# Performance work log

Measured on AMD Instinct MI355X. Metric: run time of the kernel, lower is better.

The kernel has to match this reference:

```python
import jax, jax.numpy as jnp
import numpy as np

GROUPS = 32
EPS = 1e-6

def group_norm(x, scale, bias):
    B, H, W, C = x.shape
    xg = x.reshape(B, H, W, GROUPS, C // GROUPS)
    mean = xg.mean(axis=(1, 2, 4), keepdims=True)
    var = xg.var(axis=(1, 2, 4), keepdims=True)
    xg = (xg - mean) * jax.lax.rsqrt(var + EPS)
    return xg.reshape(B, H, W, C) * scale + bias

def nin(x, w, b):
    # 1x1 dense over channel dim
    return jnp.einsum('bhwc,cd->bhwd', x, w) + b

def setup_inputs() -> dict:
    key = jax.random.key(0)
    ks = jax.random.split(key, 6)
    B, H, W, C = 8, 64, 64, 256
    s = 1.0 / np.sqrt(C)
    return {
        'x': jax.random.normal(ks[0], (B, H, W, C), jnp.float32),
        'gn_scale': jnp.ones((C,), jnp.float32),
        'gn_bias': jnp.zeros((C,), jnp.float32),
        'Wq': jax.random.normal(ks[1], (C, C), jnp.float32) * s,
        'bq': jnp.zeros((C,), jnp.float32),
        'Wk': jax.random.normal(ks[2], (C, C), jnp.float32) * s,
        'bk': jnp.zeros((C,), jnp.float32),
        'Wv': jax.random.normal(ks[3], (C, C), jnp.float32) * s,
        'bv': jnp.zeros((C,), jnp.float32),
        'Wf': jax.random.normal(ks[4], (C, C), jnp.float32) * s,
        'bf': jnp.zeros((C,), jnp.float32),
    }

def reference(x, gn_scale, gn_bias, Wq, bq, Wk, bk, Wv, bv, Wf, bf):
    B, H, W, C = x.shape
    h = group_norm(x, gn_scale, gn_bias)
    q = nin(h, Wq, bq)
    k = nin(h, Wk, bk)
    v = nin(h, Wv, bv)
    w = jnp.einsum('bhwc,bHWc->bhwHW', q, k) * (C ** -0.5)  # [B,H,W,H,W]
    w = jax.nn.softmax(w.reshape(B, H, W, H * W), axis=-1).reshape(B, H, W, H, W)
    h = jnp.einsum('bhwHW,bHWc->bhwc', w, v)
    h = nin(h, Wf, bf)
    return (x + h) / np.sqrt(2.0)  # skip_rescale=True
```

## Files before the change

### kernel.cpp

```cpp
#include <hip/hip_runtime.h>
#include <math.h>


typedef __attribute__((ext_vector_type(8))) short bf16x8;
typedef __attribute__((ext_vector_type(4))) float f32x4;
typedef __attribute__((ext_vector_type(16))) float f32x16;
typedef __attribute__((ext_vector_type(8))) int i32x8;
typedef unsigned short u16;
typedef unsigned char u8;
typedef __attribute__((address_space(3))) unsigned int lds_u32;
typedef __attribute__((address_space(1))) unsigned int glb_u32;

namespace {
constexpr int Bn = 8;
constexpr int Np = 4096;
constexpr int Cc = 256;
constexpr float kEps = 1e-6f;
constexpr float kRsqrt2 = 0.70710678118654752440f;
constexpr int kRows = Bn * Np;
}

__device__ __forceinline__ u16 f2b(float x) {
  unsigned int u = __float_as_uint(x);
  u += 0x7fffu + ((u >> 16) & 1u);
  return (u16)(u >> 16);
}

__device__ __forceinline__ u8 f2fp8(float x) {
  return (u8)(__builtin_amdgcn_cvt_pk_fp8_f32(x, x, 0, false) & 0xff);
}

__device__ __forceinline__ void stage16(const void* g, void* l) {
  __builtin_amdgcn_global_load_lds((const glb_u32*)g, (lds_u32*)l, 16, 0, 0);
}

union V8U {
  uint4 u[2];
  i32x8 v;
};

__global__ __launch_bounds__(256) void conv_w_k(
    const float* __restrict__ Wq, const float* __restrict__ Wk,
    const float* __restrict__ Wv, const float* __restrict__ Wf,
    u16* __restrict__ wsw) {
  const int w = blockIdx.x;
  const float* W = (w == 0) ? Wq : (w == 1) ? Wk : (w == 2) ? Wv : Wf;
  const int t = threadIdx.x;
  const int nt = t >> 7, r = t & 127;
  for (int c0 = 0; c0 < 32; ++c0) {
    const int c = blockIdx.y * 32 + c0;
    const float val = W[(size_t)c * Cc + t];
    const int kt = c >> 6, kk = c & 63;
    const size_t byte = (((size_t)(w * 8 + nt * 4 + kt)) << 14) +
                        (((r * 128 + kk * 2)) ^ ((r & 7) << 4));
    *(u16*)((char*)wsw + byte) = f2b(val);
  }
}

__global__ __launch_bounds__(256) void gn_stats_k(const float* __restrict__ x,
                                                  float* __restrict__ st) {
  const int bg = blockIdx.x;
  const int b = bg >> 5, g = bg & 31;
  const float* base = x + (size_t)b * Np * Cc + g * 8;
  float s = 0.f, ss = 0.f;
  for (int i = threadIdx.x; i < Np * 2; i += 256) {
    const int p = i >> 1, hh = (i & 1) * 4;
    const float4 v = *(const float4*)(base + (size_t)p * Cc + hh);
    s += v.x + v.y + v.z + v.w;
    ss += v.x * v.x + v.y * v.y + v.z * v.z + v.w * v.w;
  }
  __shared__ float red[8];
#pragma unroll
  for (int off = 32; off; off >>= 1) {
    s += __shfl_down(s, off);
    ss += __shfl_down(ss, off);
  }
  const int wid = threadIdx.x >> 6;
  if ((threadIdx.x & 63) == 0) { red[wid] = s; red[wid + 4] = ss; }
  __syncthreads();
  if (threadIdx.x == 0) {
    s = red[0] + red[1] + red[2] + red[3];
    ss = red[4] + red[5] + red[6] + red[7];
    const float mean = s * (1.f / 32768.f);
    const float var = ss * (1.f / 32768.f) - mean * mean;
    st[bg * 2] = mean;
    st[bg * 2 + 1] = rsqrtf(var + kEps);
  }
}

__global__ __launch_bounds__(256) void gn_apply_k(const float* __restrict__ x,
                                                  const float* __restrict__ st,
                                                  const float* __restrict__ gs,
                                                  const float* __restrict__ gb,
                                                  u16* __restrict__ hsw) {
  const int total = kRows * Cc / 4;
  for (int i = blockIdx.x * blockDim.x + threadIdx.x; i < total;
       i += gridDim.x * blockDim.x) {
    const int c4 = i & 63;
    const int p = i >> 6;
    const int b = p >> 12;
    const int g = c4 >> 1;
    const float mean = st[(b * 32 + g) * 2];
    const float rstd = st[(b * 32 + g) * 2 + 1];
    const float4 xv = ((const float4*)x)[i];
    const float4 sv = ((const float4*)gs)[c4];
    const float4 bv = ((const float4*)gb)[c4];
    ushort4 o;
    o.x = f2b((xv.x - mean) * rstd * sv.x + bv.x);
    o.y = f2b((xv.y - mean) * rstd * sv.y + bv.y);
    o.z = f2b((xv.z - mean) * rstd * sv.z + bv.z);
    o.w = f2b((xv.w - mean) * rstd * sv.w + bv.w);
    const int mt = p >> 7, r = p & 127;
    const int c = c4 * 4, kt = c >> 6, kk = c & 63;
    const size_t byte = (((size_t)(mt * 4 + kt)) << 14) +
                        (((r * 128 + kk * 2)) ^ ((r & 7) << 4));
    *(ushort4*)((char*)hsw + byte) = o;
  }
}

__global__ __launch_bounds__(256, 2) void gemm_k(
    const u16* __restrict__ A_sw, const u16* __restrict__ wsw,
    const float* __restrict__ bq, const float* __restrict__ bk,
    const float* __restrict__ bv, const float* __restrict__ bf,
    const float* __restrict__ x, u8* __restrict__ qg, u8* __restrict__ kg,
    u8* __restrict__ vtt, float* __restrict__ out, int mode_sel) {
  __shared__ __align__(16) u16 Al[2][8192], Bl[2][8192];
  const int mode = (mode_sel < 0) ? blockIdx.z : mode_sel;
  const int mt0 = blockIdx.x;
  const int nt0 = blockIdx.y;
  const int t = threadIdx.x;
  const int w = t >> 6, l = t & 63;
  const int wm = w >> 1, wn = w & 1;
  const int lr = l & 15, lg = l >> 4;
  f32x4 acc[4][4];
#pragma unroll
  for (int i = 0; i < 4; ++i)
#pragma unroll
    for (int j = 0; j < 4; ++j) acc[i][j] = (f32x4){0.f, 0.f, 0.f, 0.f};

  auto stg = [&](int kt, int nxt) {
    const char* at = (const char*)A_sw + (((size_t)mt0 * 4 + kt) << 14);
    const char* bt =
        (const char*)wsw + (((size_t)(mode * 8 + nt0 * 4 + kt)) << 14);
    char* ad = (char*)&Al[nxt][0];
    char* bd = (char*)&Bl[nxt][0];
#pragma unroll
    for (int p = 0; p < 4; ++p) {
      const int c = p * 256 + t;
      stage16(at + c * 16, ad + c * 16);
      stage16(bt + c * 16, bd + c * 16);
    }
  };

  stg(0, 0);
  __syncthreads();
  for (int kt = 0; kt < 4; ++kt) {
    if (kt < 3) stg(kt + 1, (kt + 1) & 1);
    const char* Ac = (const char*)&Al[kt & 1][0];
    const char* Bc = (const char*)&Bl[kt & 1][0];
    __builtin_amdgcn_s_setprio(1);
#pragma unroll
    for (int ks = 0; ks < 2; ++ks) {
      bf16x8 af[4], bfr[4];
#pragma unroll
      for (int i = 0; i < 4; ++i)
        af[i] = *(const bf16x8*)(
            Ac + (((wm * 64 + i * 16 + lr) * 128 + ks * 64 + lg * 16) ^
                  ((lr & 7) << 4)));
#pragma unroll
      for (int j = 0; j < 4; ++j)
        bfr[j] = *(const bf16x8*)(
            Bc + (((wn * 64 + j * 16 + lr) * 128 + ks * 64 + lg * 16) ^
                  ((lr & 7) << 4)));
#pragma unroll
      for (int i = 0; i < 4; ++i)
#pragma unroll
        for (int j = 0; j < 4; ++j)
          acc[i][j] = __builtin_amdgcn_mfma_f32_16x16x32_bf16(af[i], bfr[j],
                                                              acc[i][j], 0, 0, 0);
    }
    __builtin_amdgcn_s_setprio(0);
    __syncthreads();
  }
  const int m0 = mt0 * 128 + wm * 64;
  const int n0 = nt0 * 128 + wn * 64;
  const float* bias = (mode == 0) ? bq : (mode == 1) ? bk : (mode == 2) ? bv : bf;
  float bv4[4];
#pragma unroll
  for (int j = 0; j < 4; ++j) bv4[j] = bias[n0 + j * 16 + lr];
#pragma unroll
  for (int i = 0; i < 4; ++i)
#pragma unroll
    for (int e = 0; e < 4; ++e) {
      const int m = m0 + i * 16 + lg * 4 + e;
#pragma unroll
      for (int j = 0; j < 4; ++j) {
        const int n = n0 + j * 16 + lr;
        const float val = acc[i][j][e] + bv4[j];
        if (mode == 0) {
          qg[(size_t)m * Cc + n] = f2fp8(val);
        } else if (mode == 1) {
          const size_t pos = ((size_t)(m >> 6)) * 16384 +
                             ((size_t)((m >> 5) & 1)) * 8192 +
                             (n >> 6) * 2048 +
                             ((m & 31) + 32 * ((n >> 5) & 1)) * 32 + (n & 31);
          kg[pos] = f2fp8(val);
        } else if (mode == 2) {
          const int kv = m & 63;
          const size_t pos = ((size_t)(m >> 6)) * 16384 + (n >> 5) * 2048 +
                             ((n & 31) + 32 * ((kv >> 2) & 1)) * 32 +
                             (kv & 3) + 4 * ((kv & 31) >> 3) + 16 * (kv >> 5);
          vtt[pos] = f2fp8(val);
        } else {
          out[(size_t)m * Cc + n] =
              (x[(size_t)m * Cc + n] + val) * kRsqrt2;
        }
      }
    }
}

__global__ __launch_bounds__(64, 1) void attn_mfma_k(
    const u8* __restrict__ qg, const u8* __restrict__ ksw,
    const u8* __restrict__ vsw, u16* __restrict__ h2) {
  const int id = blockIdx.x;
  const int b = id & 7;
  const int qt = id >> 3;
  const int l = threadIdx.x;
  const int lq = l & 31;
  const int hi = l >> 5;

  const u8* kbase = ksw + (size_t)b * Np * Cc;
  const u8* vbase = vsw + (size_t)b * Np * Cc;

  uint4 QF[4][2];
  {
    const u8* qrow = qg + ((size_t)b * Np + qt * 32 + lq) * Cc;
#pragma unroll
    for (int m = 0; m < 4; ++m) {
      QF[m][0] = *(const uint4*)(qrow + m * 64 + hi * 32);
      QF[m][1] = *(const uint4*)(qrow + m * 64 + hi * 32 + 16);
    }
  }
  f32x16 oacc[8];
#pragma unroll
  for (int nb = 0; nb < 8; ++nb)
#pragma unroll
    for (int r = 0; r < 16; ++r) oacc[nb][r] = 0.f;
  float lrow = 0.f;

  uint4 KR[2][4][2];
  uint4 VR[8][2];

  auto loadK = [&](int gt) {
    const u8* kt = kbase + (size_t)gt * 16384;
#pragma unroll
    for (int s = 0; s < 2; ++s)
#pragma unroll
      for (int m = 0; m < 4; ++m) {
        const u8* p = kt + s * 8192 + m * 2048 + l * 32;
        KR[s][m][0] = *(const uint4*)(p);
        KR[s][m][1] = *(const uint4*)(p + 16);
      }
  };
  auto loadV = [&](int gt) {
    const u8* vt = vbase + (size_t)gt * 16384;
#pragma unroll
    for (int cb = 0; cb < 8; ++cb) {
      const u8* p = vt + cb * 2048 + l * 32;
      VR[cb][0] = *(const uint4*)(p);
      VR[cb][1] = *(const uint4*)(p + 16);
    }
  };

  loadK(0);
  loadV(0);

  for (int t = 0; t < 64; ++t) {
    f32x16 s0, s1;
#pragma unroll
    for (int r = 0; r < 16; ++r) { s0[r] = 0.f; s1[r] = 0.f; }
    __builtin_amdgcn_s_setprio(1);
#pragma unroll
    for (int m = 0; m < 4; ++m) {
      V8U ka, kb, qv;
      ka.u[0] = KR[0][m][0]; ka.u[1] = KR[0][m][1];
      kb.u[0] = KR[1][m][0]; kb.u[1] = KR[1][m][1];
      qv.u[0] = QF[m][0]; qv.u[1] = QF[m][1];
      s0 = __builtin_amdgcn_mfma_scale_f32_32x32x64_f8f6f4(
          ka.v, qv.v, s0, 0, 0, 0, 0x7F, 0, 0x7F);
      s1 = __builtin_amdgcn_mfma_scale_f32_32x32x64_f8f6f4(
          kb.v, qv.v, s1, 0, 0, 0, 0x7F, 0, 0x7F);
    }
    __builtin_amdgcn_s_setprio(0);
    if (t < 63) loadK(t + 1);
    float p0[16], p1[16];
#pragma unroll
    for (int r = 0; r < 16; ++r) {
      p0[r] = __expf(s0[r] * 0.0625f - 2.0f);
      p1[r] = __expf(s1[r] * 0.0625f - 2.0f);
    }
    lrow += ((((p0[0] + p0[1]) + (p0[2] + p0[3])) +
              ((p0[4] + p0[5]) + (p0[6] + p0[7]))) +
             (((p0[8] + p0[9]) + (p0[10] + p0[11])) +
              ((p0[12] + p0[13]) + (p0[14] + p0[15]))));
    lrow += ((((p1[0] + p1[1]) + (p1[2] + p1[3])) +
              ((p1[4] + p1[5]) + (p1[6] + p1[7]))) +
             (((p1[8] + p1[9]) + (p1[10] + p1[11])) +
              ((p1[12] + p1[13]) + (p1[14] + p1[15]))));
    V8U PP;
    unsigned int d[8];
#pragma unroll
    for (int g = 0; g < 4; ++g) {
      unsigned int r0 = (unsigned int)__builtin_amdgcn_cvt_pk_fp8_f32(
          p0[4 * g + 0], p0[4 * g + 1], 0, false);
      d[g] = (unsigned int)__builtin_amdgcn_cvt_pk_fp8_f32(
          p0[4 * g + 2], p0[4 * g + 3], (int)r0, true);
      unsigned int r1 = (unsigned int)__builtin_amdgcn_cvt_pk_fp8_f32(
          p1[4 * g + 0], p1[4 * g + 1], 0, false);
      d[4 + g] = (unsigned int)__builtin_amdgcn_cvt_pk_fp8_f32(
          p1[4 * g + 2], p1[4 * g + 3], (int)r1, true);
    }
    PP.u[0] = make_uint4(d[0], d[1], d[2], d[3]);
    PP.u[1] = make_uint4(d[4], d[5], d[6], d[7]);
    __builtin_amdgcn_s_setprio(1);
#pragma unroll
    for (int cb = 0; cb < 8; ++cb) {
      V8U vv;
      vv.u[0] = VR[cb][0]; vv.u[1] = VR[cb][1];
      oacc[cb] = __builtin_amdgcn_mfma_scale_f32_32x32x64_f8f6f4(
          vv.v, PP.v, oacc[cb], 0, 0, 0, 0x7F, 0, 0x7F);
    }
    __builtin_amdgcn_s_setprio(0);
    if (t < 63) loadV(t + 1);
  }

  lrow += __shfl_xor(lrow, 32);
  const float inv = 1.f / lrow;
  const size_t mt = (size_t)b * 32 + (qt >> 2);
  const int r = (qt & 3) * 32 + lq;
#pragma unroll
  for (int nb = 0; nb < 8; ++nb)
#pragma unroll
    for (int g = 0; g < 4; ++g) {
      const int c = nb * 32 + g * 8 + hi * 4;
      const int kt = c >> 6, kk = c & 63;
      ushort4 val;
      val.x = f2b(oacc[nb][4 * g + 0] * inv);
      val.y = f2b(oacc[nb][4 * g + 1] * inv);
      val.z = f2b(oacc[nb][4 * g + 2] * inv);
      val.w = f2b(oacc[nb][4 * g + 3] * inv);
      const size_t byte =
          ((mt * 4 + kt) << 14) + (((r * 128 + kk * 2)) ^ ((r & 7) << 4));
      *(ushort4*)((char*)h2 + byte) = val;
    }
}

extern "C" void kernel_launch(void* const* d_in, const int* in_sizes, int n_in,
                              void* d_out, int out_size, void* d_ws,
                              size_t ws_size, hipStream_t stream) {
  const float* x = (const float*)d_in[0];
  const float* gs = (const float*)d_in[1];
  const float* gb = (const float*)d_in[2];
  const float* Wq = (const float*)d_in[3];
  const float* bq = (const float*)d_in[4];
  const float* Wk = (const float*)d_in[5];
  const float* bk = (const float*)d_in[6];
  const float* Wv = (const float*)d_in[7];
  const float* bv = (const float*)d_in[8];
  const float* Wf = (const float*)d_in[9];
  const float* bf = (const float*)d_in[10];
  float* out = (float*)d_out;

  u16* hsw = (u16*)d_ws;
  u8* qg = (u8*)(hsw + (size_t)kRows * Cc);
  u8* kg = qg + (size_t)kRows * Cc;
  u8* vtt = kg + (size_t)kRows * Cc;
  u16* h2 = (u16*)(vtt + (size_t)kRows * Cc);
  u16* wsw = h2 + (size_t)kRows * Cc;
  float* st = (float*)(wsw + 4 * 8 * 8192);

  conv_w_k<<<dim3(4, 8), dim3(256), 0, stream>>>(Wq, Wk, Wv, Wf, wsw);
  gn_stats_k<<<dim3(Bn * 32), dim3(256), 0, stream>>>(x, st);
  gn_apply_k<<<dim3(1024), dim3(256), 0, stream>>>(x, st, gs, gb, hsw);
  gemm_k<<<dim3(kRows / 128, Cc / 128, 3), dim3(256), 0, stream>>>(
      hsw, wsw, bq, bk, bv, bf, x, qg, kg, vtt, out, -1);
  attn_mfma_k<<<dim3(1024), dim3(64), 0, stream>>>(qg, kg, vtt, h2);
  gemm_k<<<dim3(kRows / 128, Cc / 128, 1), dim3(256), 0, stream>>>(
      h2, wsw, bq, bk, bv, bf, x, qg, kg, vtt, out, 3);
}
```

Baseline: 199.8 us.

## Fuse group-norm stats/apply and software-pipeline QK with PV in attention

The group-norm statistics and apply kernels are merged into one kernel per (batch, group) that reduces and then re-reads its slice to write bf16 swizzled output. This removes a launch and the stats round-trip, but the fused kernel runs with only 256 blocks. The attention loop is restructured into a two-stage software pipeline with double-buffered K registers, so the QK MFMA for the next tile overlaps the softmax and PV of the current one. The cost is higher register pressure, which could spill at the one-wave occupancy.

Result: slower. 236.5 us (+18.4%).

```diff
diff --git a/kernel.cpp b/kernel.cpp
--- a/kernel.cpp
+++ b/kernel.cpp
@@ -57,64 +57,68 @@
   }
 }
 
-__global__ __launch_bounds__(256) void gn_stats_k(const float* __restrict__ x,
-                                                  float* __restrict__ st) {
+__global__ __launch_bounds__(256) void gn_fused_k(const float* __restrict__ x,
+                                                  const float* __restrict__ gs,
+                                                  const float* __restrict__ gb,
+                                                  u16* __restrict__ hsw) {
   const int bg = blockIdx.x;
   const int b = bg >> 5, g = bg & 31;
   const float* base = x + (size_t)b * Np * Cc + g * 8;
+  const int t = threadIdx.x;
   float s = 0.f, ss = 0.f;
-  for (int i = threadIdx.x; i < Np * 2; i += 256) {
-    const int p = i >> 1, hh = (i & 1) * 4;
-    const float4 v = *(const float4*)(base + (size_t)p * Cc + hh);
-    s += v.x + v.y + v.z + v.w;
-    ss += v.x * v.x + v.y * v.y + v.z * v.z + v.w * v.w;
-  }
-  __shared__ float red[8];
+#pragma unroll
+  for (int i = 0; i < 16; ++i) {
+    const int p = i * 256 + t;
+    const float4 a = *(const float4*)(base + (size_t)p * Cc);
+    const float4 c = *(const float4*)(base + (size_t)p * Cc + 4);
+    s += (a.x + a.y) + (a.z + a.w) + (c.x + c.y) + (c.z + c.w);
+    ss += a.x * a.x + a.y * a.y + a.z * a.z + a.w * a.w +
+          c.x * c.x + c.y * c.y + c.z * c.z + c.w * c.w;
+  }
+  __shared__ float red[16];
 #pragma unroll
   for (int off = 32; off; off >>= 1) {
-    s += __shfl_down(s, off);
-    ss += __shfl_down(ss, off);
-  }
-  const int wid = threadIdx.x >> 6;
-  if ((threadIdx.x & 63) == 0) { red[wid] = s; red[wid + 4] = ss; }
+    s += __shfl_xor(s, off);
+    ss += __shfl_xor(ss, off);
+  }
+  if ((t & 63) == 0) { red[t >> 6] = s; red[8 + (t >> 6)] = ss; }
   __syncthreads();
-  if (threadIdx.x == 0) {
-    s = red[0] + red[1] + red[2] + red[3];
-    ss = red[4] + red[5] + red[6] + red[7];
-    const float mean = s * (1.f / 32768.f);
-    const float var = ss * (1.f / 32768.f) - mean * mean;
-    st[bg * 2] = mean;
-    st[bg * 2 + 1] = rsqrtf(var + kEps);
-  }
-}
-
-__global__ __launch_bounds__(256) void gn_apply_k(const float* __restrict__ x,
-                                                  const float* __restrict__ st,
-                                                  const float* __restrict__ gs,
-                                                  const float* __restrict__ gb,
-                                                  u16* __restrict__ hsw) {
-  const int total = kRows * Cc / 4;
-  for (int i = blockIdx.x * blockDim.x + threadIdx.x; i < total;
-       i += gridDim.x * blockDim.x) {
-    const int c4 = i & 63;
-    const int p = i >> 6;
-    const int b = p >> 12;
-    const int g = c4 >> 1;
-    const float mean = st[(b * 32 + g) * 2];
-    const float rstd = st[(b * 32 + g) * 2 + 1];
-    const float4 xv = ((const float4*)x)[i];
-    const float4 sv = ((const float4*)gs)[c4];
-    const float4 bv = ((const float4*)gb)[c4];
-    ushort4 o;
-    o.x = f2b((xv.x - mean) * rstd * sv.x + bv.x);
-    o.y = f2b((xv.y - mean) * rstd * sv.y + bv.y);
-    o.z = f2b((xv.z - mean) * rstd * sv.z + bv.z);
-    o.w = f2b((xv.w - mean) * rstd * sv.w + bv.w);
-    const int mt = p >> 7, r = p & 127;
-    const int c = c4 * 4, kt = c >> 6, kk = c & 63;
+  s = (red[0] + red[1]) + (red[2] + red[3]);
+  ss = (red[8] + red[9]) + (red[10] + red[11]);
+  const float mean = s * (1.f / 32768.f);
+  const float rstd = rsqrtf(ss * (1.f / 32768.f) - mean * mean + kEps);
+  float sv[8], bv[8];
+  {
+    const float4 s0 = *(const float4*)(gs + g * 8);
+    const float4 s1 = *(const float4*)(gs + g * 8 + 4);
+    const float4 b0 = *(const float4*)(gb + g * 8);
+    const float4 b1 = *(const float4*)(gb + g * 8 + 4);
+    sv[0] = s0.x; sv[1] = s0.y; sv[2] = s0.z; sv[3] = s0.w;
+    sv[4] = s1.x; sv[5] = s1.y; sv[6] = s1.z; sv[7] = s1.w;
+    bv[0] = b0.x; bv[1] = b0.y; bv[2] = b0.z; bv[3] = b0.w;
+    bv[4] = b1.x; bv[5] = b1.y; bv[6] = b1.z; bv[7] = b1.w;
+  }
+  const int kt = g >> 3;
+  const int koff = (g & 7) * 16;
+#pragma unroll
+  for (int i = 0; i < 16; ++i) {
+    const int p = i * 256 + t;
+    const float4 a = *(const float4*)(base + (size_t)p * Cc);
+    const float4 c = *(const float4*)(base + (size_t)p * Cc + 4);
+    union { u16 h[8]; uint4 q; } o;
+    o.h[0] = f2b((a.x - mean) * rstd * sv[0] + bv[0]);
+    o.h[1] = f2b((a.y - mean) * rstd * sv[1] + bv[1]);
+    o.h[2] = f2b((a.z - mean) * rstd * sv[2] + bv[2]);
+    o.h[3] = f2b((a.w - mean) * rstd * sv[3] + bv[3]);
+    o.h[4] = f2b((c.x - mean) * rstd * sv[4] + bv[4]);
+    o.h[5] = f2b((c.y - mean) * rstd * sv[5] + bv[5]);
+    o.h[6] = f2b((c.z - mean) * rstd * sv[6] + bv[6]);
+    o.h[7] = f2b((c.w - mean) * rstd * sv[7] + bv[7]);
+    const size_t row = (size_t)b * Np + p;
+    const int mt = (int)(row >> 7), r = (int)(row & 127);
     const size_t byte = (((size_t)(mt * 4 + kt)) << 14) +
-                        (((r * 128 + kk * 2)) ^ ((r & 7) << 4));
-    *(ushort4*)((char*)hsw + byte) = o;
+                        (((r * 128 + koff)) ^ ((r & 7) << 4));
+    *(uint4*)((char*)hsw + byte) = o.q;
   }
 }
 
@@ -232,13 +236,15 @@
   const u8* kbase = ksw + (size_t)b * Np * Cc;
   const u8* vbase = vsw + (size_t)b * Np * Cc;
 
-  uint4 QF[4][2];
+  i32x8 QF[4];
   {
     const u8* qrow = qg + ((size_t)b * Np + qt * 32 + lq) * Cc;
 #pragma unroll
     for (int m = 0; m < 4; ++m) {
-      QF[m][0] = *(const uint4*)(qrow + m * 64 + hi * 32);
-      QF[m][1] = *(const uint4*)(qrow + m * 64 + hi * 32 + 16);
+      V8U u;
+      u.u[0] = *(const uint4*)(qrow + m * 64 + hi * 32);
+      u.u[1] = *(const uint4*)(qrow + m * 64 + hi * 32 + 16);
+      QF[m] = u.v;
     }
   }
   f32x16 oacc[8];
@@ -248,90 +254,109 @@
     for (int r = 0; r < 16; ++r) oacc[nb][r] = 0.f;
   float lrow = 0.f;
 
-  uint4 KR[2][4][2];
-  uint4 VR[8][2];
-
-  auto loadK = [&](int gt) {
+  i32x8 KA[8], KB[8], VRr[8];
+
+  auto loadK = [&](int gt, i32x8* K) {
     const u8* kt = kbase + (size_t)gt * 16384;
 #pragma unroll
-    for (int s = 0; s < 2; ++s)
-#pragma unroll
-      for (int m = 0; m < 4; ++m) {
-        const u8* p = kt + s * 8192 + m * 2048 + l * 32;
-        KR[s][m][0] = *(const uint4*)(p);
-        KR[s][m][1] = *(const uint4*)(p + 16);
-      }
+    for (int i = 0; i < 8; ++i) {
+      const u8* p = kt + (i >> 2) * 8192 + (i & 3) * 2048 + l * 32;
+      V8U u;
+      u.u[0] = *(const uint4*)(p);
+      u.u[1] = *(const uint4*)(p + 16);
+      K[i] = u.v;
+    }
   };
   auto loadV = [&](int gt) {
     const u8* vt = vbase + (size_t)gt * 16384;
 #pragma unroll
     for (int cb = 0; cb < 8; ++cb) {
       const u8* p = vt + cb * 2048 + l * 32;
-      VR[cb][0] = *(const uint4*)(p);
-      VR[cb][1] = *(const uint4*)(p + 16);
-    }
-  };
-
-  loadK(0);
-  loadV(0);
-
-  for (int t = 0; t < 64; ++t) {
-    f32x16 s0, s1;
+      V8U u;
+      u.u[0] = *(const uint4*)(p);
+      u.u[1] = *(const uint4*)(p + 16);
+      VRr[cb] = u.v;
+    }
+  };
+
+  auto qk = [&](const i32x8* K, f32x16& s0, f32x16& s1) {
 #pragma unroll
     for (int r = 0; r < 16; ++r) { s0[r] = 0.f; s1[r] = 0.f; }
     __builtin_amdgcn_s_setprio(1);
 #pragma unroll
     for (int m = 0; m < 4; ++m) {
-      V8U ka, kb, qv;
-      ka.u[0] = KR[0][m][0]; ka.u[1] = KR[0][m][1];
-      kb.u[0] = KR[1][m][0]; kb.u[1] = KR[1][m][1];
-      qv.u[0] = QF[m][0]; qv.u[1] = QF[m][1];
       s0 = __builtin_amdgcn_mfma_scale_f32_32x32x64_f8f6f4(
-          ka.v, qv.v, s0, 0, 0, 0, 0x7F, 0, 0x7F);
+          K[m], QF[m], s0, 0, 0, 0, 0x7F, 0, 0x7F);
       s1 = __builtin_amdgcn_mfma_scale_f32_32x32x64_f8f6f4(
-          kb.v, qv.v, s1, 0, 0, 0, 0x7F, 0, 0x7F);
+          K[4 + m], QF[m], s1, 0, 0, 0, 0x7F, 0, 0x7F);
     }
     __builtin_amdgcn_s_setprio(0);
-    if (t < 63) loadK(t + 1);
-    float p0[16], p1[16];
-#pragma unroll
-    for (int r = 0; r < 16; ++r) {
-      p0[r] = __expf(s0[r] * 0.0625f - 2.0f);
-      p1[r] = __expf(s1[r] * 0.0625f - 2.0f);
-    }
-    lrow += ((((p0[0] + p0[1]) + (p0[2] + p0[3])) +
-              ((p0[4] + p0[5]) + (p0[6] + p0[7]))) +
-             (((p0[8] + p0[9]) + (p0[10] + p0[11])) +
-              ((p0[12] + p0[13]) + (p0[14] + p0[15]))));
-    lrow += ((((p1[0] + p1[1]) + (p1[2] + p1[3])) +
-              ((p1[4] + p1[5]) + (p1[6] + p1[7]))) +
-             (((p1[8] + p1[9]) + (p1[10] + p1[11])) +
-              ((p1[12] + p1[13]) + (p1[14] + p1[15]))));
-    V8U PP;
+  };
+
+  auto smpack = [&](const f32x16& s0, const f32x16& s1, V8U& PP) {
     unsigned int d[8];
 #pragma unroll
     for (int g = 0; g < 4; ++g) {
+      const float a0 = __expf(s0[4 * g + 0] * 0.0625f - 2.0f);
+      const float a1 = __expf(s0[4 * g + 1] * 0.0625f - 2.0f);
+      const float a2 = __expf(s0[4 * g + 2] * 0.0625f - 2.0f);
+      const float a3 = __expf(s0[4 * g + 3] * 0.0625f - 2.0f);
+      lrow += (a0 + a1) + (a2 + a3);
       unsigned int r0 = (unsigned int)__builtin_amdgcn_cvt_pk_fp8_f32(
-          p0[4 * g + 0], p0[4 * g + 1], 0, false);
-      d[g] = (unsigned int)__builtin_amdgcn_cvt_pk_fp8_f32(
-          p0[4 * g + 2], p0[4 * g + 3], (int)r0, true);
+          a0, a1, 0, false);
+      d[g] = (unsigned int)__builtin_amdgcn_cvt_pk_fp8_f32(a2, a3, (int)r0,
+                                                           true);
+      const float b0 = __expf(s1[4 * g + 0] * 0.0625f - 2.0f);
+      const float b1 = __expf(s1[4 * g + 1] * 0.0625f - 2.0f);
+      const float b2 = __expf(s1[4 * g + 2] * 0.0625f - 2.0f);
+      const float b3 = __expf(s1[4 * g + 3] * 0.0625f - 2.0f);
+      lrow += (b0 + b1) + (b2 + b3);
       unsigned int r1 = (unsigned int)__builtin_amdgcn_cvt_pk_fp8_f32(
-          p1[4 * g + 0], p1[4 * g + 1], 0, false);
-      d[4 + g] = (unsigned int)__builtin_amdgcn_cvt_pk_fp8_f32(
-          p1[4 * g + 2], p1[4 * g + 3], (int)r1, true);
+          b0, b1, 0, false);
+      d[4 + g] = (unsigned int)__builtin_amdgcn_cvt_pk_fp8_f32(b2, b3, (int)r1,
+                                                               true);
     }
     PP.u[0] = make_uint4(d[0], d[1], d[2], d[3]);
     PP.u[1] = make_uint4(d[4], d[5], d[6], d[7]);
+  };
+
+  auto pv = [&](const V8U& PP) {
     __builtin_amdgcn_s_setprio(1);
 #pragma unroll
     for (int cb = 0; cb < 8; ++cb) {
-      V8U vv;
-      vv.u[0] = VR[cb][0]; vv.u[1] = VR[cb][1];
       oacc[cb] = __builtin_amdgcn_mfma_scale_f32_32x32x64_f8f6f4(
-          vv.v, PP.v, oacc[cb], 0, 0, 0, 0x7F, 0, 0x7F);
+          VRr[cb], PP.v, oacc[cb], 0, 0, 0, 0x7F, 0, 0x7F);
     }
     __builtin_amdgcn_s_setprio(0);
-    if (t < 63) loadV(t + 1);
+  };
+
+  f32x16 sA0, sA1, sB0, sB1;
+  loadK(0, KA);
+  loadV(0);
+  qk(KA, sA0, sA1);
+  loadK(1, KB);
+
+  for (int t = 0; t <= 60; t += 2) {
+    V8U PP;
+    smpack(sA0, sA1, PP);
+    qk(KB, sB0, sB1);
+    pv(PP);
+    loadV(t + 1);
+    loadK(t + 2, KA);
+    smpack(sB0, sB1, PP);
+    qk(KA, sA0, sA1);
+    pv(PP);
+    loadV(t + 2);
+    loadK(t + 3, KB);
+  }
+  {
+    V8U PP;
+    smpack(sA0, sA1, PP);
+    qk(KB, sB0, sB1);
+    pv(PP);
+    loadV(63);
+    smpack(sB0, sB1, PP);
+    pv(PP);
   }
 
   lrow += __shfl_xor(lrow, 32);
@@ -377,11 +402,9 @@
   u8* vtt = kg + (size_t)kRows * Cc;
   u16* h2 = (u16*)(vtt + (size_t)kRows * Cc);
   u16* wsw = h2 + (size_t)kRows * Cc;
-  float* st = (float*)(wsw + 4 * 8 * 8192);
 
   conv_w_k<<<dim3(4, 8), dim3(256), 0, stream>>>(Wq, Wk, Wv, Wf, wsw);
-  gn_stats_k<<<dim3(Bn * 32), dim3(256), 0, stream>>>(x, st);
-  gn_apply_k<<<dim3(1024), dim3(256), 0, stream>>>(x, st, gs, gb, hsw);
+  gn_fused_k<<<dim3(256), dim3(256), 0, stream>>>(x, gs, gb, hsw);
   gemm_k<<<dim3(kRows / 128, Cc / 128, 3), dim3(256), 0, stream>>>(
       hsw, wsw, bq, bk, bv, bf, x, qg, kg, vtt, out, -1);
   attn_mfma_k<<<dim3(1024), dim3(64), 0, stream>>>(qg, kg, vtt, h2);
```

## Software-pipeline attention loop: overlap next QK MFMA with softmax of current tile

Applied to the files above, without the earlier changes.

Restructures the attention inner loop into a two-stage software pipeline. The QK^T MFMAs for the next key tile are issued between the softmax/pack of the current tile and its PV MFMAs, so exp work can overlap matrix-core work. K tiles are double-buffered in registers. exp is rewritten as exp2 with a fused scale and shift, and loads use 32-byte vector types. The extra K buffer and score accumulators raise register pressure in a kernel that already runs one wave per block.

Result: slower. 301.3 us (+50.8%).

```diff
diff --git a/kernel.cpp b/kernel.cpp
--- a/kernel.cpp
+++ b/kernel.cpp
@@ -18,7 +18,15 @@
 constexpr float kEps = 1e-6f;
 constexpr float kRsqrt2 = 0.70710678118654752440f;
 constexpr int kRows = Bn * Np;
-}
+constexpr float kSc2 = 1.44269504088896340736f / 16.0f;
+constexpr float kSh2 = -2.0f * 1.44269504088896340736f;
+}
+
+#if __has_builtin(__builtin_amdgcn_exp2f)
+#define EXP2F(x) __builtin_amdgcn_exp2f(x)
+#else
+#define EXP2F(x) exp2f(x)
+#endif
 
 __device__ __forceinline__ u16 f2b(float x) {
   unsigned int u = __float_as_uint(x);
@@ -33,11 +41,6 @@
 __device__ __forceinline__ void stage16(const void* g, void* l) {
   __builtin_amdgcn_global_load_lds((const glb_u32*)g, (lds_u32*)l, 16, 0, 0);
 }
-
-union V8U {
-  uint4 u[2];
-  i32x8 v;
-};
 
 __global__ __launch_bounds__(256) void conv_w_k(
     const float* __restrict__ Wq, const float* __restrict__ Wk,
@@ -232,14 +235,12 @@
   const u8* kbase = ksw + (size_t)b * Np * Cc;
   const u8* vbase = vsw + (size_t)b * Np * Cc;
 
-  uint4 QF[4][2];
+  i32x8 QF[4];
   {
     const u8* qrow = qg + ((size_t)b * Np + qt * 32 + lq) * Cc;
 #pragma unroll
-    for (int m = 0; m < 4; ++m) {
-      QF[m][0] = *(const uint4*)(qrow + m * 64 + hi * 32);
-      QF[m][1] = *(const uint4*)(qrow + m * 64 + hi * 32 + 16);
-    }
+    for (int m = 0; m < 4; ++m)
+      QF[m] = *(const i32x8*)(qrow + m * 64 + hi * 32);
   }
   f32x16 oacc[8];
 #pragma unroll
@@ -248,90 +249,90 @@
     for (int r = 0; r < 16; ++r) oacc[nb][r] = 0.f;
   float lrow = 0.f;
 
-  uint4 KR[2][4][2];
-  uint4 VR[8][2];
-
-  auto loadK = [&](int gt) {
+  i32x8 KA[8], KB[8], VRr[8];
+
+  auto loadK = [&](int gt, i32x8* K) {
     const u8* kt = kbase + (size_t)gt * 16384;
 #pragma unroll
-    for (int s = 0; s < 2; ++s)
-#pragma unroll
-      for (int m = 0; m < 4; ++m) {
-        const u8* p = kt + s * 8192 + m * 2048 + l * 32;
-        KR[s][m][0] = *(const uint4*)(p);
-        KR[s][m][1] = *(const uint4*)(p + 16);
-      }
+    for (int i = 0; i < 8; ++i)
+      K[i] = *(const i32x8*)(kt + (i >> 2) * 8192 + (i & 3) * 2048 + l * 32);
   };
   auto loadV = [&](int gt) {
     const u8* vt = vbase + (size_t)gt * 16384;
 #pragma unroll
+    for (int cb = 0; cb < 8; ++cb)
+      VRr[cb] = *(const i32x8*)(vt + cb * 2048 + l * 32);
+  };
+
+  auto qk = [&](const i32x8* K, f32x16& s0, f32x16& s1) {
+#pragma unroll
+    for (int r = 0; r < 16; ++r) { s0[r] = 0.f; s1[r] = 0.f; }
+#pragma unroll
+    for (int m = 0; m < 4; ++m) {
+      s0 = __builtin_amdgcn_mfma_scale_f32_32x32x64_f8f6f4(
+          K[m], QF[m], s0, 0, 0, 0, 0x7F, 0, 0x7F);
+      s1 = __builtin_amdgcn_mfma_scale_f32_32x32x64_f8f6f4(
+          K[4 + m], QF[m], s1, 0, 0, 0, 0x7F, 0, 0x7F);
+    }
+  };
+
+  auto smpack = [&](const f32x16& s0, const f32x16& s1, i32x8& PP) {
+#pragma unroll
+    for (int g = 0; g < 4; ++g) {
+      const float a0 = EXP2F(fmaf(s0[4 * g + 0], kSc2, kSh2));
+      const float a1 = EXP2F(fmaf(s0[4 * g + 1], kSc2, kSh2));
+      const float a2 = EXP2F(fmaf(s0[4 * g + 2], kSc2, kSh2));
+      const float a3 = EXP2F(fmaf(s0[4 * g + 3], kSc2, kSh2));
+      lrow += (a0 + a1) + (a2 + a3);
+      unsigned int r0 = (unsigned int)__builtin_amdgcn_cvt_pk_fp8_f32(
+          a0, a1, 0, false);
+      PP[g] = __builtin_amdgcn_cvt_pk_fp8_f32(a2, a3, (int)r0, true);
+      const float b0 = EXP2F(fmaf(s1[4 * g + 0], kSc2, kSh2));
+      const float b1 = EXP2F(fmaf(s1[4 * g + 1], kSc2, kSh2));
+      const float b2 = EXP2F(fmaf(s1[4 * g + 2], kSc2, kSh2));
+      const float b3 = EXP2F(fmaf(s1[4 * g + 3], kSc2, kSh2));
+      lrow += (b0 + b1) + (b2 + b3);
+      unsigned int r1 = (unsigned int)__builtin_amdgcn_cvt_pk_fp8_f32(
+          b0, b1, 0, false);
+      PP[4 + g] = __builtin_amdgcn_cvt_pk_fp8_f32(b2, b3, (int)r1, true);
+    }
+  };
+
+  auto pv = [&](const i32x8& PP) {
+#pragma unroll
     for (int cb = 0; cb < 8; ++cb) {
-      const u8* p = vt + cb * 2048 + l * 32;
-      VR[cb][0] = *(const uint4*)(p);
-      VR[cb][1] = *(const uint4*)(p + 16);
-    }
-  };
-
-  loadK(0);
+      oacc[cb] = __builtin_amdgcn_mfma_scale_f32_32x32x64_f8f6f4(
+          VRr[cb], PP, oacc[cb], 0, 0, 0, 0x7F, 0, 0x7F);
+    }
+  };
+
+  f32x16 sA0, sA1, sB0, sB1;
+  loadK(0, KA);
   loadV(0);
-
-  for (int t = 0; t < 64; ++t) {
-    f32x16 s0, s1;
-#pragma unroll
-    for (int r = 0; r < 16; ++r) { s0[r] = 0.f; s1[r] = 0.f; }
-    __builtin_amdgcn_s_setprio(1);
-#pragma unroll
-    for (int m = 0; m < 4; ++m) {
-      V8U ka, kb, qv;
-      ka.u[0] = KR[0][m][0]; ka.u[1] = KR[0][m][1];
-      kb.u[0] = KR[1][m][0]; kb.u[1] = KR[1][m][1];
-      qv.u[0] = QF[m][0]; qv.u[1] = QF[m][1];
-      s0 = __builtin_amdgcn_mfma_scale_f32_32x32x64_f8f6f4(
-          ka.v, qv.v, s0, 0, 0, 0, 0x7F, 0, 0x7F);
-      s1 = __builtin_amdgcn_mfma_scale_f32_32x32x64_f8f6f4(
-          kb.v, qv.v, s1, 0, 0, 0, 0x7F, 0, 0x7F);
-    }
-    __builtin_amdgcn_s_setprio(0);
-    if (t < 63) loadK(t + 1);
-    float p0[16], p1[16];
-#pragma unroll
-    for (int r = 0; r < 16; ++r) {
-      p0[r] = __expf(s0[r] * 0.0625f - 2.0f);
-      p1[r] = __expf(s1[r] * 0.0625f - 2.0f);
-    }
-    lrow += ((((p0[0] + p0[1]) + (p0[2] + p0[3])) +
-              ((p0[4] + p0[5]) + (p0[6] + p0[7]))) +
-             (((p0[8] + p0[9]) + (p0[10] + p0[11])) +
-              ((p0[12] + p0[13]) + (p0[14] + p0[15]))));
-    lrow += ((((p1[0] + p1[1]) + (p1[2] + p1[3])) +
-              ((p1[4] + p1[5]) + (p1[6] + p1[7]))) +
-             (((p1[8] + p1[9]) + (p1[10] + p1[11])) +
-              ((p1[12] + p1[13]) + (p1[14] + p1[15]))));
-    V8U PP;
-    unsigned int d[8];
-#pragma unroll
-    for (int g = 0; g < 4; ++g) {
-      unsigned int r0 = (unsigned int)__builtin_amdgcn_cvt_pk_fp8_f32(
-          p0[4 * g + 0], p0[4 * g + 1], 0, false);
-      d[g] = (unsigned int)__builtin_amdgcn_cvt_pk_fp8_f32(
-          p0[4 * g + 2], p0[4 * g + 3], (int)r0, true);
-      unsigned int r1 = (unsigned int)__builtin_amdgcn_cvt_pk_fp8_f32(
-          p1[4 * g + 0], p1[4 * g + 1], 0, false);
-      d[4 + g] = (unsigned int)__builtin_amdgcn_cvt_pk_fp8_f32(
-          p1[4 * g + 2], p1[4 * g + 3], (int)r1, true);
-    }
-    PP.u[0] = make_uint4(d[0], d[1], d[2], d[3]);
-    PP.u[1] = make_uint4(d[4], d[5], d[6], d[7]);
-    __builtin_amdgcn_s_setprio(1);
-#pragma unroll
-    for (int cb = 0; cb < 8; ++cb) {
-      V8U vv;
-      vv.u[0] = VR[cb][0]; vv.u[1] = VR[cb][1];
-      oacc[cb] = __builtin_amdgcn_mfma_scale_f32_32x32x64_f8f6f4(
-          vv.v, PP.v, oacc[cb], 0, 0, 0, 0x7F, 0, 0x7F);
-    }
-    __builtin_amdgcn_s_setprio(0);
-    if (t < 63) loadV(t + 1);
+  qk(KA, sA0, sA1);
+  loadK(1, KB);
+
+  for (int t = 0; t <= 60; t += 2) {
+    i32x8 PP;
+    smpack(sA0, sA1, PP);
+    qk(KB, sB0, sB1);
+    pv(PP);
+    loadV(t + 1);
+    loadK(t + 2, KA);
+    smpack(sB0, sB1, PP);
+    qk(KA, sA0, sA1);
+    pv(PP);
+    loadV(t + 2);
+    loadK(t + 3, KB);
+  }
+  {
+    i32x8 PP;
+    smpack(sA0, sA1, PP);
+    qk(KB, sB0, sB1);
+    pv(PP);
+    loadV(63);
+    smpack(sB0, sB1, PP);
+    pv(PP);
   }
 
   lrow += __shfl_xor(lrow, 32);
```
